# Kernel tuning notes

Hardware: AMD Instinct MI355X
Metric: run time of the kernel (lower is better)

The kernel has to match this reference:

```python
import jax, jax.numpy as jnp
import numpy as np

STRIDE = 4
H, W, A = 208, 336, 3
ANCHOR_SCALE = 8.0
ASPECTS = ((1.0, 1.0), (1.4, 0.7), (0.7, 1.4))  # (aspect_x, aspect_y)
PRE_NMS = 2000
POST_NMS = 1000
IOU_THR = 0.7
BBOX_CLIP = float(np.log(1000.0 / 16.0))


def make_anchors():
    # EfficientDet/SageMakerCV-style anchors at level 2, boxes as (y1, x1, y2, x2)
    base = ANCHOR_SCALE * STRIDE  # 32
    yc = (np.arange(H, dtype=np.float32) + 0.5) * STRIDE
    xc = (np.arange(W, dtype=np.float32) + 0.5) * STRIDE
    yy, xx = np.meshgrid(yc, xc, indexing='ij')  # [H, W]
    per_aspect = []
    for ax, ay in ASPECTS:
        hx, hy = base * ax / 2.0, base * ay / 2.0
        per_aspect.append(np.stack([yy - hy, xx - hx, yy + hy, xx + hx], axis=-1))
    return np.stack(per_aspect, axis=2).reshape(-1, 4).astype(np.float32)  # [H*W*A, 4]


def decode(deltas, anchors):
    # deltas: [B, N, 4] (dy, dx, dh, dw); anchors: [N, 4]; weights (1,1,1,1)
    ah = anchors[:, 2] - anchors[:, 0]
    aw = anchors[:, 3] - anchors[:, 1]
    acy = anchors[:, 0] + 0.5 * ah
    acx = anchors[:, 1] + 0.5 * aw
    dy, dx = deltas[..., 0], deltas[..., 1]
    dh = jnp.clip(deltas[..., 2], -BBOX_CLIP, BBOX_CLIP)
    dw = jnp.clip(deltas[..., 3], -BBOX_CLIP, BBOX_CLIP)
    cy = dy * ah + acy
    cx = dx * aw + acx
    h = jnp.exp(dh) * ah
    w = jnp.exp(dw) * aw
    return jnp.stack([cy - 0.5 * h, cx - 0.5 * w, cy + 0.5 * h, cx + 0.5 * w], axis=-1)


def _iou_one_to_many(box, boxes):
    y1 = jnp.maximum(box[0], boxes[:, 0])
    x1 = jnp.maximum(box[1], boxes[:, 1])
    y2 = jnp.minimum(box[2], boxes[:, 2])
    x2 = jnp.minimum(box[3], boxes[:, 3])
    inter = jnp.maximum(y2 - y1, 0.0) * jnp.maximum(x2 - x1, 0.0)
    a1 = (box[2] - box[0]) * (box[3] - box[1])
    a2 = (boxes[:, 2] - boxes[:, 0]) * (boxes[:, 3] - boxes[:, 1])
    return inter / (a1 + a2 - inter + 1e-8)


def nms_single(boxes, scores):
    # greedy NMS, fixed POST_NMS iterations (jit-friendly)
    def body(i, state):
        sc, kb, ks = state
        j = jnp.argmax(sc)
        b, s = boxes[j], sc[j]
        kb = kb.at[i].set(b)
        ks = ks.at[i].set(s)
        sup = _iou_one_to_many(b, boxes) > IOU_THR  # suppresses j itself (iou=1)
        sc = jnp.where(sup, -1.0, sc)
        return sc, kb, ks

    init = (scores,
            jnp.zeros((POST_NMS, 4), boxes.dtype),
            jnp.zeros((POST_NMS,), scores.dtype))
    _, kb, ks = jax.lax.fori_loop(0, POST_NMS, body, init)
    return kb, ks


def setup_inputs() -> dict:
    key = jax.random.key(0)
    k0, k1, k2 = jax.random.split(key, 3)
    feats = jax.random.normal(k0, (2, H, W, 256), dtype=jnp.float32)
    img_info = jnp.ones((2, 2), jnp.float32) * jnp.array([832.0, 1344.0], jnp.float32)
    w_cls = 0.01 * jax.random.normal(k1, (256, A * 1), dtype=jnp.float32)
    b_cls = jnp.zeros((A * 1,), jnp.float32)
    w_reg = 0.01 * jax.random.normal(k2, (256, A * 4), dtype=jnp.float32)
    b_reg = jnp.zeros((A * 4,), jnp.float32)
    return {"feats": feats, "img_info": img_info, "w_cls": w_cls, "b_cls": b_cls,
            "w_reg": w_reg, "b_reg": b_reg}


def reference(feats, img_info, w_cls, b_cls, w_reg, b_reg):
    B = feats.shape[0]
    # 1x1 convs == channel matmuls
    cls_scores = jnp.einsum('bhwc,co->bhwo', feats, w_cls) + b_cls  # [B,H,W,3]
    bbox_preds = jnp.einsum('bhwc,co->bhwo', feats, w_reg) + b_reg  # [B,H,W,12]

    scores = jax.nn.sigmoid(cls_scores).reshape(B, -1)       # [B, N]
    deltas = bbox_preds.reshape(B, -1, 4)                    # [B, N, 4]
    anchors = jnp.asarray(make_anchors())                    # [N, 4]
    boxes = decode(deltas, anchors)                          # [B, N, 4]

    # clip to image extents
    hmax = img_info[:, 0][:, None]
    wmax = img_info[:, 1][:, None]
    boxes = jnp.stack([
        jnp.clip(boxes[..., 0], 0.0, hmax),
        jnp.clip(boxes[..., 1], 0.0, wmax),
        jnp.clip(boxes[..., 2], 0.0, hmax),
        jnp.clip(boxes[..., 3], 0.0, wmax)], axis=-1)

    # per-image pre-NMS topk
    top_s, idx = jax.lax.top_k(scores, PRE_NMS)              # [B, PRE]
    top_b = jnp.take_along_axis(boxes, idx[..., None], axis=1)  # [B, PRE, 4]

    rois, roi_scores = jax.vmap(nms_single)(top_b, top_s)    # [B, POST, 4], [B, POST]
    return cls_scores, bbox_preds, rois, roi_scores
```

## Files before the change

kernel.cpp:

```cpp
#include <hip/hip_runtime.h>
#include <cstdint>
#include <cstddef>

#define HH 208
#define WW 336
#define NA 3
#define NPER 209664
#define NROWS 139776
#define NB 2
#define PRE_K 2000
#define POST_K 1000
#define CAP 8192
#define MW 32
#define MROWS 2048
#define BBOX_CLIP_F 4.135166556742356f

#define WS_HIST   0
#define WS_HIST2  32768
#define WS_META   65536
#define WS_META24 65544
#define WS_CCNT   65552
#define WS_KEEPW  65568
#define WS_CAND   66080
#define WS_SBOX   197152
#define WS_SSC    261152
#define WS_MASK   277248
#define WS_ZERO_WORDS 49288

__device__ __forceinline__ float sigmoidf_ref(float x) {
  return __fdiv_rn(1.0f, __fadd_rn(1.0f, expf(-x)));
}
__device__ __forceinline__ unsigned int score_u(float logit) {
  float s = sigmoidf_ref(logit);
  return __float_as_uint(s) | 0x80000000u;
}

__device__ __forceinline__ unsigned long long bcast64(unsigned long long v, int l) {
  unsigned int lo = (unsigned int)__builtin_amdgcn_readlane((int)(unsigned int)v, l);
  unsigned int hi = (unsigned int)__builtin_amdgcn_readlane((int)(unsigned int)(v >> 32), l);
  return ((unsigned long long)hi << 32) | lo;
}

__device__ __forceinline__ float4 decode_box(const float* __restrict__ bbox,
                                             int b, unsigned int n,
                                             float hmax, float wmax) {
  unsigned int a = n % 3u;
  unsigned int pix = n / 3u;
  unsigned int y = pix / (unsigned int)WW;
  unsigned int x = pix % (unsigned int)WW;
  float yc = ((float)y + 0.5f) * 4.0f;
  float xc = ((float)x + 0.5f) * 4.0f;
  float hx = (a == 0) ? 16.0f : ((a == 1) ? 22.4f : 11.2f);
  float hy = (a == 0) ? 16.0f : ((a == 1) ? 11.2f : 22.4f);
  float ay1 = __fsub_rn(yc, hy), ax1 = __fsub_rn(xc, hx);
  float ay2 = __fadd_rn(yc, hy), ax2 = __fadd_rn(xc, hx);
  float ah = __fsub_rn(ay2, ay1), aw = __fsub_rn(ax2, ax1);
  float acy = __fadd_rn(ay1, __fmul_rn(0.5f, ah));
  float acx = __fadd_rn(ax1, __fmul_rn(0.5f, aw));
  const float* d = bbox + ((size_t)b * NPER + n) * 4u;
  float dy = d[0], dx = d[1];
  float dh = fminf(fmaxf(d[2], -BBOX_CLIP_F), BBOX_CLIP_F);
  float dw = fminf(fmaxf(d[3], -BBOX_CLIP_F), BBOX_CLIP_F);
  float cy = __fadd_rn(__fmul_rn(dy, ah), acy);
  float cx = __fadd_rn(__fmul_rn(dx, aw), acx);
  float hh = __fmul_rn(expf(dh), ah);
  float wwv = __fmul_rn(expf(dw), aw);
  float y1 = __fsub_rn(cy, __fmul_rn(0.5f, hh));
  float x1 = __fsub_rn(cx, __fmul_rn(0.5f, wwv));
  float y2 = __fadd_rn(cy, __fmul_rn(0.5f, hh));
  float x2 = __fadd_rn(cx, __fmul_rn(0.5f, wwv));
  y1 = fminf(fmaxf(y1, 0.0f), hmax);
  x1 = fminf(fmaxf(x1, 0.0f), wmax);
  y2 = fminf(fmaxf(y2, 0.0f), hmax);
  x2 = fminf(fmaxf(x2, 0.0f), wmax);
  return make_float4(y1, x1, y2, x2);
}

__device__ __forceinline__ float iou_ref(float4 bi, float4 bj) {
  float yA = fmaxf(bi.x, bj.x);
  float xA = fmaxf(bi.y, bj.y);
  float yB = fminf(bi.z, bj.z);
  float xB = fminf(bi.w, bj.w);
  float inter = __fmul_rn(fmaxf(__fsub_rn(yB, yA), 0.0f),
                          fmaxf(__fsub_rn(xB, xA), 0.0f));
  float a1 = __fmul_rn(__fsub_rn(bi.z, bi.x), __fsub_rn(bi.w, bi.y));
  float a2 = __fmul_rn(__fsub_rn(bj.z, bj.x), __fsub_rn(bj.w, bj.y));
  float den = __fadd_rn(__fsub_rn(__fadd_rn(a1, a2), inter), 1e-8f);
  return __fdiv_rn(inter, den);
}

__global__ void k_zero(unsigned int* __restrict__ p, int n) {
  int i = blockIdx.x * blockDim.x + threadIdx.x;
  if (i < n) p[i] = 0u;
}

__global__ __launch_bounds__(256) void k_head(
    const float* __restrict__ feats, const float* __restrict__ w_cls,
    const float* __restrict__ b_cls, const float* __restrict__ w_reg,
    const float* __restrict__ b_reg, float* __restrict__ out_cls,
    float* __restrict__ out_bbox) {
  const int lane = threadIdx.x & 63;
  const int wid = blockIdx.x * (blockDim.x >> 6) + (threadIdx.x >> 6);
  const int nw = gridDim.x * (blockDim.x >> 6);
  const int k0 = lane << 2;
  const int l15 = lane & 15;
  const int ol = ((l15 & 1) << 3) | ((l15 & 2) << 1) | ((l15 & 4) >> 1) |
                 ((l15 & 8) >> 3);

  float wreg[4][16];
#pragma unroll
  for (int j = 0; j < 16; ++j) {
    const int o = ol ^ j;
#pragma unroll
    for (int kk = 0; kk < 4; ++kk) {
      wreg[kk][j] = (o < 3) ? w_cls[(k0 + kk) * 3 + o]
                            : (o < 15 ? w_reg[(k0 + kk) * 12 + (o - 3)] : 0.0f);
    }
  }
  const float bias = (ol < 3) ? b_cls[ol] : (ol < 15 ? b_reg[ol - 3] : 0.0f);

  for (int r = wid; r < NROWS; r += nw) {
    const float4 f4 = *(const float4*)(feats + (size_t)r * 256 + k0);
    float a[16];
#pragma unroll
    for (int j = 0; j < 16; ++j) {
      a[j] = f4.x * wreg[0][j];
      a[j] += f4.y * wreg[1][j];
      a[j] += f4.z * wreg[2][j];
      a[j] += f4.w * wreg[3][j];
    }
#pragma unroll
    for (int s = 0; s < 8; ++s) a[s] += __shfl_xor(a[8 + s], 1, 64);
#pragma unroll
    for (int s = 0; s < 4; ++s) a[s] += __shfl_xor(a[4 + s], 2, 64);
#pragma unroll
    for (int s = 0; s < 2; ++s) a[s] += __shfl_xor(a[2 + s], 4, 64);
    a[0] += __shfl_xor(a[1], 8, 64);
    a[0] += __shfl_xor(a[0], 16, 64);
    a[0] += __shfl_xor(a[0], 32, 64);
    if (lane < 16 && ol < 15) {
      float v = a[0] + bias;
      if (ol < 3) out_cls[(size_t)r * 3 + ol] = v;
      else        out_bbox[(size_t)r * 12 + (ol - 3)] = v;
    }
  }
}

__global__ __launch_bounds__(256) void k_hist(const float* __restrict__ out_cls,
                                              unsigned int* __restrict__ hist) {
  const int b = blockIdx.y;
  __shared__ unsigned int h[4096];
  for (int i = threadIdx.x; i < 4096; i += blockDim.x) h[i] = 0u;
  __syncthreads();
  for (int i = blockIdx.x * blockDim.x + threadIdx.x; i < NPER;
       i += gridDim.x * blockDim.x) {
    unsigned int u = score_u(out_cls[(size_t)b * NPER + i]);
    atomicAdd(&h[u >> 20], 1u);
  }
  __syncthreads();
  for (int i = threadIdx.x; i < 4096; i += blockDim.x)
    if (h[i]) atomicAdd(&hist[b * 4096 + i], h[i]);
}

__global__ __launch_bounds__(1024) void k_thresh(const unsigned int* __restrict__ hist,
                                                 unsigned int* __restrict__ meta_T) {
  const int b = blockIdx.x;
  const int t = threadIdx.x;
  __shared__ unsigned int sums[1024];
  unsigned int hb[4];
  unsigned int s = 0u;
#pragma unroll
  for (int q = 0; q < 4; ++q) {
    int bin = 4095 - (t * 4 + q);
    hb[q] = hist[b * 4096 + bin];
    s += hb[q];
  }
  sums[t] = s;
  __syncthreads();
  for (int off = 1; off < 1024; off <<= 1) {
    unsigned int v = (t >= off) ? sums[t - off] : 0u;
    __syncthreads();
    sums[t] += v;
    __syncthreads();
  }
  unsigned int excl = sums[t] - s;
  if (excl < PRE_K && excl + s >= PRE_K) {
    unsigned int c = excl;
#pragma unroll
    for (int q = 0; q < 4; ++q) {
      c += hb[q];
      if (c >= PRE_K) { meta_T[b] = (unsigned int)(4095 - (t * 4 + q)); break; }
    }
  }
}

__global__ __launch_bounds__(256) void k_hist2(const float* __restrict__ out_cls,
                                               const unsigned int* __restrict__ meta_T,
                                               unsigned int* __restrict__ hist2) {
  const int b = blockIdx.y;
  const unsigned int T = meta_T[b];
  __shared__ unsigned int h[4096];
  for (int i = threadIdx.x; i < 4096; i += blockDim.x) h[i] = 0u;
  __syncthreads();
  for (int i = blockIdx.x * blockDim.x + threadIdx.x; i < NPER;
       i += gridDim.x * blockDim.x) {
    unsigned int u = score_u(out_cls[(size_t)b * NPER + i]);
    if ((u >> 20) == T) atomicAdd(&h[(u >> 8) & 0xFFFu], 1u);
  }
  __syncthreads();
  for (int i = threadIdx.x; i < 4096; i += blockDim.x)
    if (h[i]) atomicAdd(&hist2[b * 4096 + i], h[i]);
}

__global__ __launch_bounds__(1024) void k_thresh2(const unsigned int* __restrict__ hist,
                                                  const unsigned int* __restrict__ hist2,
                                                  const unsigned int* __restrict__ meta_T,
                                                  unsigned int* __restrict__ meta_T24) {
  const int b = blockIdx.x;
  const int t = threadIdx.x;
  const unsigned int T = meta_T[b];
  __shared__ unsigned int sums[1024];
  __shared__ unsigned int c0s;
  unsigned int c0 = 0u;
  for (int i = t; i < 4096; i += 1024)
    if ((unsigned int)i > T) c0 += hist[b * 4096 + i];
  sums[t] = c0;
  __syncthreads();
  for (int off = 512; off > 0; off >>= 1) {
    if (t < off) sums[t] += sums[t + off];
    __syncthreads();
  }
  if (t == 0) c0s = sums[0];
  __syncthreads();
  const unsigned int C0 = c0s;
  __syncthreads();
  unsigned int hb[4];
  unsigned int s = 0u;
#pragma unroll
  for (int q = 0; q < 4; ++q) {
    int bin = 4095 - (t * 4 + q);
    hb[q] = hist2[b * 4096 + bin];
    s += hb[q];
  }
  sums[t] = s;
  __syncthreads();
  for (int off = 1; off < 1024; off <<= 1) {
    unsigned int v = (t >= off) ? sums[t - off] : 0u;
    __syncthreads();
    sums[t] += v;
    __syncthreads();
  }
  unsigned int excl = sums[t] - s;
  if (C0 + excl < PRE_K && C0 + excl + s >= PRE_K) {
    unsigned int c = C0 + excl;
#pragma unroll
    for (int q = 0; q < 4; ++q) {
      c += hb[q];
      if (c >= PRE_K) {
        meta_T24[b] = (T << 12) | (unsigned int)(4095 - (t * 4 + q));
        break;
      }
    }
  }
}

__global__ __launch_bounds__(256) void k_compact(const float* __restrict__ out_cls,
                                                 const unsigned int* __restrict__ meta_T24,
                                                 unsigned int* __restrict__ cand_count,
                                                 unsigned long long* __restrict__ cand) {
  const int b = blockIdx.y;
  const unsigned int T24 = meta_T24[b];
  for (int i = blockIdx.x * blockDim.x + threadIdx.x; i < NPER;
       i += gridDim.x * blockDim.x) {
    unsigned int u = score_u(out_cls[(size_t)b * NPER + i]);
    if ((u >> 8) >= T24) {
      unsigned int pos = atomicAdd(&cand_count[b], 1u);
      if (pos < CAP)
        cand[(size_t)b * CAP + pos] =
            ((unsigned long long)u << 32) | (unsigned int)(~(unsigned int)i);
    }
  }
}

__global__ __launch_bounds__(1024) void k_sort(const unsigned long long* __restrict__ cand,
                                               const unsigned int* __restrict__ cand_count,
                                               const float* __restrict__ out_bbox,
                                               const float* __restrict__ img_info,
                                               float* __restrict__ sboxes,
                                               float* __restrict__ sscores) {
  const int b = blockIdx.x;
  const int t = threadIdx.x;
  __shared__ unsigned long long keys[CAP];
  unsigned int cc = cand_count[b];
  if (cc > CAP) cc = CAP;
  int n = 2048;
  while ((unsigned int)n < cc) n <<= 1;
  for (int i = t; i < n; i += 1024) keys[i] = cand[(size_t)b * CAP + i];
  __syncthreads();
  for (int k = 2; k <= n; k <<= 1) {
    for (int j = k >> 1; j > 0; j >>= 1) {
      for (int i = t; i < n; i += 1024) {
        int ixj = i ^ j;
        if (ixj > i) {
          unsigned long long a = keys[i], c = keys[ixj];
          bool up = ((i & k) == 0);
          bool sw = up ? (a < c) : (a > c);
          if (sw) { keys[i] = c; keys[ixj] = a; }
        }
      }
      __syncthreads();
    }
  }
  const float hmax = img_info[b * 2 + 0];
  const float wmax = img_info[b * 2 + 1];
  for (int i = t; i < PRE_K; i += 1024) {
    unsigned long long key = keys[i];
    unsigned int u = (unsigned int)(key >> 32);
    unsigned int idx = ~(unsigned int)(key & 0xFFFFFFFFull);
    float sc = __uint_as_float(u & 0x7FFFFFFFu);
    float4 bx = decode_box(out_bbox, b, idx, hmax, wmax);
    ((float4*)sboxes)[(size_t)b * PRE_K + i] = bx;
    sscores[(size_t)b * PRE_K + i] = sc;
  }
}

__global__ __launch_bounds__(64) void k_mask(const float* __restrict__ sboxes,
                                             unsigned long long* __restrict__ mask) {
  const int b = blockIdx.z;
  const int rb = blockIdx.x;
  const int cb = blockIdx.y;
  const int t = threadIdx.x;
  __shared__ float4 cbox[64];
  const int col0 = cb * 64;
  {
    int c = col0 + t;
    cbox[t] = (c < PRE_K) ? ((const float4*)sboxes)[(size_t)b * PRE_K + c]
                          : make_float4(0.f, 0.f, 0.f, 0.f);
  }
  __syncthreads();
  const int i = rb * 64 + t;
  if (i >= PRE_K) return;
  float4 bi = ((const float4*)sboxes)[(size_t)b * PRE_K + i];
  unsigned long long bits = 0ull;
#pragma unroll 8
  for (int j = 0; j < 64; ++j) {
    int c = col0 + j;
    if (c > i && c < PRE_K) {
      if (iou_ref(bi, cbox[j]) > 0.7f) bits |= (1ull << j);
    }
  }
  mask[((size_t)b * MROWS + i) * MW + cb] = bits;
}

#define MLOAD(BUF, G)                                                     \
  {                                                                       \
    _Pragma("unroll") for (int _k = 0; _k < 32; ++_k) {                   \
      int _row = (G) * 64 + 2 * _k + psel;                                \
      (BUF)[_k] = (_row < PRE_K) ? M[(size_t)(G) * 2048 + 64 * _k + lane] \
                                 : 0ull;                                  \
    }                                                                     \
  }
#define DLOAD(DST, G)                                                     \
  {                                                                       \
    int _row = (G) * 64 + lane;                                           \
    (DST) = ((G) < 32 && _row < PRE_K) ? M[(size_t)_row * MW + (G)] : 0ull; \
  }
#define GSTEP(G, MCUR, MNEXT, DCUR, DNEXT)                                \
  do {                                                                    \
    MLOAD(MNEXT, (G) + 1);                                                \
    DLOAD(DNEXT, (G) + 1);                                                \
    unsigned long long w = bcast64(remv, (G)) | bcast64(remv, (G) + 32);  \
    unsigned long long alive = ~w;                                        \
    if ((G) == 31) alive &= (1ull << (PRE_K - 31 * 64)) - 1ull;           \
    unsigned long long kept = 0ull;                                       \
    while (alive) {                                                       \
      int j = __builtin_ctzll(alive);                                     \
      unsigned long long bit = 1ull << j;                                 \
      kept |= bit;                                                        \
      unsigned long long dj = bcast64((DCUR), j);                         \
      alive &= ~(dj | bit);                                               \
    }                                                                     \
    int pc = __popcll(kept);                                              \
    if (nk + pc >= POST_K) {                                              \
      int need = POST_K - nk;                                             \
      unsigned long long k2 = kept;                                       \
      for (int _t = 0; _t < need; ++_t) k2 &= k2 - 1;                     \
      kept ^= k2;                \
      if (lane == 0) keepw[b * 32 + (G)] = kept;                          \
      stop = 1;                                                           \
    } else {                                                              \
      nk += pc;                                                           \
      if (lane == 0) keepw[b * 32 + (G)] = kept;                          \
      unsigned long long keptv = kept >> psel;                            \
      _Pragma("unroll") for (int _q = 0; _q < 32; ++_q) {                 \
        unsigned long long sel = 0ull - ((keptv >> (2 * _q)) & 1ull);     \
        remv |= (MCUR)[_q] & sel;                                         \
      }                                                                   \
    }                                                                     \
  } while (0)

__global__ __launch_bounds__(64, 1) void k_scan(
    const unsigned long long* __restrict__ mask,
    unsigned long long* __restrict__ keepw) {
  const int b = blockIdx.x;
  const int lane = threadIdx.x;
  const int psel = lane >> 5;
  const unsigned long long* M = mask + (size_t)b * MROWS * MW;

  unsigned long long mbA[32], mbB[32], dA, dB;
  unsigned long long remv = 0ull;
  int nk = 0, stop = 0;

  MLOAD(mbA, 0);
  DLOAD(dA, 0);
  for (int g = 0; g < 32; g += 2) {
    GSTEP(g, mbA, mbB, dA, dB);
    if (stop) break;
    GSTEP(g + 1, mbB, mbA, dB, dA);
    if (stop) break;
  }
}

__global__ __launch_bounds__(64) void k_write(const float* __restrict__ sboxes,
                                              const float* __restrict__ sscores,
                                              const unsigned long long* __restrict__ keepw,
                                              float* __restrict__ rois,
                                              float* __restrict__ rsc) {
  const int b = blockIdx.x;
  const int lane = threadIdx.x;
  unsigned long long w = (lane < 32) ? keepw[b * 32 + lane] : 0ull;
  int pc = __popcll(w);
  int pref = pc;
#pragma unroll
  for (int off = 1; off < 64; off <<= 1) {
    int v = __shfl_up(pref, off, 64);
    if (lane >= off) pref += v;
  }
  const int excl = pref - pc;
  const int Ktot = __shfl(pref, 63, 64);
  int rank = excl;
  unsigned long long ww = w;
  while (ww) {
    int j = __builtin_ctzll(ww);
    ww &= ww - 1;
    int row = lane * 64 + j;
    ((float4*)rois)[(size_t)b * POST_K + rank] =
        ((const float4*)sboxes)[(size_t)b * PRE_K + row];
    rsc[(size_t)b * POST_K + rank] = sscores[(size_t)b * PRE_K + row];
    ++rank;
  }
  float4 pad = ((const float4*)sboxes)[(size_t)b * PRE_K + 0];
  for (int i = Ktot + lane; i < POST_K; i += 64) {
    ((float4*)rois)[(size_t)b * POST_K + i] = pad;
    rsc[(size_t)b * POST_K + i] = -1.0f;
  }
}

extern "C" void kernel_launch(void* const* d_in, const int* in_sizes, int n_in,
                              void* d_out, int out_size, void* d_ws, size_t ws_size,
                              hipStream_t stream) {
  const float* feats    = (const float*)d_in[0];
  const float* img_info = (const float*)d_in[1];
  const float* w_cls    = (const float*)d_in[2];
  const float* b_cls    = (const float*)d_in[3];
  const float* w_reg    = (const float*)d_in[4];
  const float* b_reg    = (const float*)d_in[5];

  float* out = (float*)d_out;
  float* out_cls  = out;
  float* out_bbox = out + 419328;
  float* out_rois = out + 2096640;
  float* out_rsc  = out + 2104640;

  char* ws = (char*)d_ws;
  unsigned int* hist        = (unsigned int*)(ws + WS_HIST);
  unsigned int* hist2       = (unsigned int*)(ws + WS_HIST2);
  unsigned int* meta_T      = (unsigned int*)(ws + WS_META);
  unsigned int* meta_T24    = (unsigned int*)(ws + WS_META24);
  unsigned int* cand_count  = (unsigned int*)(ws + WS_CCNT);
  unsigned long long* keepw = (unsigned long long*)(ws + WS_KEEPW);
  unsigned long long* cand  = (unsigned long long*)(ws + WS_CAND);
  float* sboxes             = (float*)(ws + WS_SBOX);
  float* sscores            = (float*)(ws + WS_SSC);
  unsigned long long* mask  = (unsigned long long*)(ws + WS_MASK);

  k_zero<<<(WS_ZERO_WORDS + 255) / 256, 256, 0, stream>>>((unsigned int*)ws, WS_ZERO_WORDS);
  k_head<<<2048, 256, 0, stream>>>(feats, w_cls, b_cls, w_reg, b_reg, out_cls, out_bbox);
  k_hist<<<dim3(128, NB), 256, 0, stream>>>(out_cls, hist);
  k_thresh<<<NB, 1024, 0, stream>>>(hist, meta_T);
  k_hist2<<<dim3(128, NB), 256, 0, stream>>>(out_cls, meta_T, hist2);
  k_thresh2<<<NB, 1024, 0, stream>>>(hist, hist2, meta_T, meta_T24);
  k_compact<<<dim3(128, NB), 256, 0, stream>>>(out_cls, meta_T24, cand_count, cand);
  k_sort<<<NB, 1024, 0, stream>>>(cand, cand_count, out_bbox, img_info, sboxes, sscores);
  k_mask<<<dim3(32, 32, NB), 64, 0, stream>>>(sboxes, mask);
  k_scan<<<NB, 64, 0, stream>>>(mask, keepw);
  k_write<<<NB, 64, 0, stream>>>(sboxes, sscores, keepw, out_rois, out_rsc);
}
```

Baseline: 412.4 us.

## Fuse score histogram into head kernel and skip lower-triangle mask work

Moves the first-pass score histogram into the 1x1-conv head kernel so each block bins its own sigmoid scores in shared memory as it writes them, which removes the separate k_hist kernel and its re-read of the class logits. The head grid is split per image so each block feeds a single image's histogram. The workspace zeroing shrinks to the counters, with k_sort padding unused key slots itself and k_mask writing zeros for lower-triangle tiles and returning early instead of computing IoU. The head kernel now carries a 16KB shared histogram and contended atomics, which may cost occupancy.

```diff
diff --git a/kernel.cpp b/kernel.cpp
--- a/kernel.cpp
+++ b/kernel.cpp
@@ -7,6 +7,7 @@
 #define NA 3
 #define NPER 209664
 #define NROWS 139776
+#define RPI 69888
 #define NB 2
 #define PRE_K 2000
 #define POST_K 1000
@@ -25,7 +26,7 @@
 #define WS_SBOX   197152
 #define WS_SSC    261152
 #define WS_MASK   277248
-#define WS_ZERO_WORDS 49288
+#define WS_ZERO_WORDS 16520
 
 __device__ __forceinline__ float sigmoidf_ref(float x) {
   return __fdiv_rn(1.0f, __fadd_rn(1.0f, expf(-x)));
@@ -98,7 +99,8 @@
     const float* __restrict__ feats, const float* __restrict__ w_cls,
     const float* __restrict__ b_cls, const float* __restrict__ w_reg,
     const float* __restrict__ b_reg, float* __restrict__ out_cls,
-    float* __restrict__ out_bbox) {
+    float* __restrict__ out_bbox, unsigned int* __restrict__ hist) {
+  const int b = blockIdx.y;
   const int lane = threadIdx.x & 63;
   const int wid = blockIdx.x * (blockDim.x >> 6) + (threadIdx.x >> 6);
   const int nw = gridDim.x * (blockDim.x >> 6);
@@ -107,6 +109,10 @@
   const int ol = ((l15 & 1) << 3) | ((l15 & 2) << 1) | ((l15 & 4) >> 1) |
                  ((l15 & 8) >> 3);
 
+  __shared__ unsigned int h[4096];
+  for (int i = threadIdx.x; i < 4096; i += blockDim.x) h[i] = 0u;
+  __syncthreads();
+
   float wreg[4][16];
 #pragma unroll
   for (int j = 0; j < 16; ++j) {
@@ -119,7 +125,8 @@
   }
   const float bias = (ol < 3) ? b_cls[ol] : (ol < 15 ? b_reg[ol - 3] : 0.0f);
 
-  for (int r = wid; r < NROWS; r += nw) {
+  for (int rr = wid; rr < RPI; rr += nw) {
+    const int r = b * RPI + rr;
     const float4 f4 = *(const float4*)(feats + (size_t)r * 256 + k0);
     float a[16];
 #pragma unroll
@@ -140,22 +147,13 @@
     a[0] += __shfl_xor(a[0], 32, 64);
     if (lane < 16 && ol < 15) {
       float v = a[0] + bias;
-      if (ol < 3) out_cls[(size_t)r * 3 + ol] = v;
-      else        out_bbox[(size_t)r * 12 + (ol - 3)] = v;
-    }
-  }
-}
-
-__global__ __launch_bounds__(256) void k_hist(const float* __restrict__ out_cls,
-                                              unsigned int* __restrict__ hist) {
-  const int b = blockIdx.y;
-  __shared__ unsigned int h[4096];
-  for (int i = threadIdx.x; i < 4096; i += blockDim.x) h[i] = 0u;
-  __syncthreads();
-  for (int i = blockIdx.x * blockDim.x + threadIdx.x; i < NPER;
-       i += gridDim.x * blockDim.x) {
-    unsigned int u = score_u(out_cls[(size_t)b * NPER + i]);
-    atomicAdd(&h[u >> 20], 1u);
+      if (ol < 3) {
+        out_cls[(size_t)r * 3 + ol] = v;
+        atomicAdd(&h[score_u(v) >> 20], 1u);
+      } else {
+        out_bbox[(size_t)r * 12 + (ol - 3)] = v;
+      }
+    }
   }
   __syncthreads();
   for (int i = threadIdx.x; i < 4096; i += blockDim.x)
@@ -295,7 +293,8 @@
   if (cc > CAP) cc = CAP;
   int n = 2048;
   while ((unsigned int)n < cc) n <<= 1;
-  for (int i = t; i < n; i += 1024) keys[i] = cand[(size_t)b * CAP + i];
+  for (int i = t; i < n; i += 1024)
+    keys[i] = (i < (int)cc) ? cand[(size_t)b * CAP + i] : 0ull;
   __syncthreads();
   for (int k = 2; k <= n; k <<= 1) {
     for (int j = k >> 1; j > 0; j >>= 1) {
@@ -330,6 +329,11 @@
   const int rb = blockIdx.x;
   const int cb = blockIdx.y;
   const int t = threadIdx.x;
+  if (cb < rb) {
+    int i = rb * 64 + t;
+    if (i < PRE_K) mask[((size_t)b * MROWS + i) * MW + cb] = 0ull;
+    return;
+  }
   __shared__ float4 cbox[64];
   const int col0 = cb * 64;
   {
@@ -485,8 +489,8 @@
   unsigned long long* mask  = (unsigned long long*)(ws + WS_MASK);
 
   k_zero<<<(WS_ZERO_WORDS + 255) / 256, 256, 0, stream>>>((unsigned int*)ws, WS_ZERO_WORDS);
-  k_head<<<2048, 256, 0, stream>>>(feats, w_cls, b_cls, w_reg, b_reg, out_cls, out_bbox);
-  k_hist<<<dim3(128, NB), 256, 0, stream>>>(out_cls, hist);
+  k_head<<<dim3(1024, NB), 256, 0, stream>>>(feats, w_cls, b_cls, w_reg, b_reg,
+                                             out_cls, out_bbox, hist);
   k_thresh<<<NB, 1024, 0, stream>>>(hist, meta_T);
   k_hist2<<<dim3(128, NB), 256, 0, stream>>>(out_cls, meta_T, hist2);
   k_thresh2<<<NB, 1024, 0, stream>>>(hist, hist2, meta_T, meta_T24);
```

Result: no change. 414.7 us (+0.6%).
